# Optimization experiments

Hardware: AMD Instinct MI355X
Metric: run time of the kernel (lower is better)

Reference implementation:

```python
import jax, jax.numpy as jnp
import numpy as np

N0, N1, E, B = 100000, 100000, 800000, 1024
F0, F1 = 93, 43


def _gin(x, src, dst, w, b, n):
    # GINConv(eps=0): h_i = Lin(x_i + sum_{j->i} x_j)
    agg = jax.ops.segment_sum(x[src], dst, num_segments=n)
    return (x + agg) @ w + b


def _pool(x, batch, num_graphs):
    s = jax.ops.segment_sum(x, batch, num_segments=num_graphs)
    cnt = jax.ops.segment_sum(jnp.ones((x.shape[0],), x.dtype), batch, num_segments=num_graphs)
    mean = s / jnp.maximum(cnt, 1.0)[:, None]
    mx = jax.ops.segment_max(x, batch, num_segments=num_graphs)
    return jnp.concatenate([mean, mx], axis=1)


def _pairnorm(x, eps=1e-5):
    x = x - x.mean(axis=0, keepdims=True)
    return x / jnp.sqrt(eps + (x * x).sum(-1).mean())


def _bn(x, gamma, beta, eps=1e-5):
    mu = x.mean(axis=0, keepdims=True)
    var = x.var(axis=0, keepdims=True)
    return (x - mu) / jnp.sqrt(var + eps) * gamma + beta


def _branch(x, ei, batch, n, wc_a, bc_a, wc_b, bc_b, fg_w1, fg_b1, fg_w2, fg_b2, fg_g, fg_bt, ff_w1, ff_b1, ff_w2, ff_b2):
    src, dst = ei[0], ei[1]
    h = jax.nn.relu(_gin(x, src, dst, wc_a, bc_a, n))
    h = jax.nn.relu(_gin(h, src, dst, wc_b, bc_b, n))
    g = _pairnorm(_pool(h, batch, B))
    g = jax.nn.relu(g @ fg_w1 + fg_b1)
    g = _bn(g @ fg_w2 + fg_b2, fg_g, fg_bt)  # [B, 512]
    z = jax.nn.relu(g @ ff_w1 + ff_b1)
    z = jax.nn.sigmoid(z @ ff_w2 + ff_b2)  # [B, 2]
    return z[:, 0], z[:, 1], g


def setup_inputs() -> dict:
    key = jax.random.key(0)
    ks = iter(jax.random.split(key, 40))

    def lin(fan_in, fan_out):
        bnd = 1.0 / np.sqrt(fan_in)
        w = jax.random.uniform(next(ks), (fan_in, fan_out), jnp.float32, -bnd, bnd)
        b = jax.random.uniform(next(ks), (fan_out,), jnp.float32, -bnd, bnd)
        return w, b

    x0 = jax.random.normal(next(ks), (N0, F0), jnp.float32)
    x1 = jax.random.normal(next(ks), (N1, F1), jnp.float32)
    ei0 = jax.random.randint(next(ks), (2, E), 0, N0, jnp.int32)
    ei1 = jax.random.randint(next(ks), (2, E), 0, N1, jnp.int32)
    b0 = jnp.sort(jax.random.randint(next(ks), (N0,), 0, B, jnp.int32))
    b1 = jnp.sort(jax.random.randint(next(ks), (N1,), 0, B, jnp.int32))

    inp = {"x0": x0, "edge_index_0": ei0, "batch_0": b0, "x1": x1, "edge_index_1": ei1, "batch_1": b1}
    inp["w_c1"], inp["b_c1"] = lin(F0, F0)
    inp["w_c2"], inp["b_c2"] = lin(F0, F0 * 10)
    inp["w_c3"], inp["b_c3"] = lin(F1, F1)
    inp["w_c4"], inp["b_c4"] = lin(F1, F1 * 10)
    inp["fg0_w1"], inp["fg0_b1"] = lin(F0 * 10 * 2, 1024)
    inp["fg0_w2"], inp["fg0_b2"] = lin(1024, 512)
    inp["fg0_g"], inp["fg0_bt"] = jnp.ones((512,), jnp.float32), jnp.zeros((512,), jnp.float32)
    inp["fg1_w1"], inp["fg1_b1"] = lin(F1 * 10 * 2, 1024)
    inp["fg1_w2"], inp["fg1_b2"] = lin(1024, 512)
    inp["fg1_g"], inp["fg1_bt"] = jnp.ones((512,), jnp.float32), jnp.zeros((512,), jnp.float32)
    inp["ff0_w1"], inp["ff0_b1"] = lin(512, 256)
    inp["ff0_w2"], inp["ff0_b2"] = lin(256, 2)
    inp["ff1_w1"], inp["ff1_b1"] = lin(512, 256)
    inp["ff1_w2"], inp["ff1_b2"] = lin(256, 2)
    return inp


def reference(x0, edge_index_0, batch_0, x1, edge_index_1, batch_1,
              w_c1, b_c1, w_c2, b_c2, w_c3, b_c3, w_c4, b_c4,
              fg0_w1, fg0_b1, fg0_w2, fg0_b2, fg0_g, fg0_bt,
              fg1_w1, fg1_b1, fg1_w2, fg1_b2, fg1_g, fg1_bt,
              ff0_w1, ff0_b1, ff0_w2, ff0_b2,
              ff1_w1, ff1_b1, ff1_w2, ff1_b2):
    alpha, beta, xg0 = _branch(x0, edge_index_0, batch_0, N0, w_c1, b_c1, w_c2, b_c2,
                               fg0_w1, fg0_b1, fg0_w2, fg0_b2, fg0_g, fg0_bt,
                               ff0_w1, ff0_b1, ff0_w2, ff0_b2)
    alpha1, beta1, xg1 = _branch(x1, edge_index_1, batch_1, N1, w_c3, b_c3, w_c4, b_c4,
                                 fg1_w1, fg1_b1, fg1_w2, fg1_b2, fg1_g, fg1_bt,
                                 ff1_w1, ff1_b1, ff1_w2, ff1_b2)
    return (alpha, beta, xg0, xg1, alpha1, beta1)
```

## Files before the change

### kernel.cpp

```cpp
#include <hip/hip_runtime.h>
#include <hip/hip_bf16.h>
#include <math.h>

#define EDGES 800000
#define NNODES 100000
#define NGRAPH 1024

typedef __attribute__((ext_vector_type(8))) short short8v;
typedef __attribute__((ext_vector_type(4))) float float4v;
typedef unsigned short ushort_t;

__device__ inline ushort_t f2bf(float f) {
  __hip_bfloat16 h = __float2bfloat16(f);
  return *reinterpret_cast<ushort_t*>(&h);
}
__device__ inline float bf2f(ushort_t u) {
  return __uint_as_float(((unsigned int)u) << 16);
}

#define NBMAX 512

__global__ __launch_bounds__(256) void bcount_k(const int* __restrict__ dst,
                                                int* __restrict__ bcnt, int E,
                                                int NB) {
  __shared__ int hist[NBMAX];
  int t = threadIdx.x;
  for (int b = t; b < NB; b += 256) hist[b] = 0;
  __syncthreads();
  int e0 = blockIdx.x * 4096;
  int e1 = min(E, e0 + 4096);
  for (int e = e0 + t; e < e1; e += 256) atomicAdd(&hist[dst[e] >> 8], 1);
  __syncthreads();
  for (int b = t; b < NB; b += 256)
    if (hist[b] > 0) atomicAdd(&bcnt[b], hist[b]);
}

__global__ __launch_bounds__(512) void bscan_k(const int* __restrict__ bcnt,
                                               int* __restrict__ boff, int NB) {
  __shared__ int tmp[512];
  int t = threadIdx.x;
  int v = (t < NB) ? bcnt[t] : 0;
  tmp[t] = v;
  __syncthreads();
  for (int off = 1; off < 512; off <<= 1) {
    int x = (t >= off) ? tmp[t - off] : 0;
    __syncthreads();
    tmp[t] += x;
    __syncthreads();
  }
  if (t < NB) boff[t] = tmp[t] - v;
  if (t == NB - 1) boff[NB] = tmp[t];
}

__global__ __launch_bounds__(256) void bscatter_k(const int* __restrict__ src,
                                                  const int* __restrict__ dst,
                                                  const int* __restrict__ boff,
                                                  int* __restrict__ bcur,
                                                  int2* __restrict__ EB, int E,
                                                  int NB) {
  __shared__ int hist[NBMAX], run[NBMAX], lcur[NBMAX];
  int t = threadIdx.x;
  for (int b = t; b < NB; b += 256) {
    hist[b] = 0;
    lcur[b] = 0;
  }
  __syncthreads();
  int e0 = blockIdx.x * 4096;
  int e1 = min(E, e0 + 4096);
  for (int e = e0 + t; e < e1; e += 256) atomicAdd(&hist[dst[e] >> 8], 1);
  __syncthreads();
  for (int b = t; b < NB; b += 256)
    if (hist[b] > 0) run[b] = atomicAdd(&bcur[b], hist[b]);
  __syncthreads();
  for (int e = e0 + t; e < e1; e += 256) {
    int d = dst[e];
    int b = d >> 8;
    int l = atomicAdd(&lcur[b], 1);
    int pos = boff[b] + run[b] + l;
    EB[pos] = make_int2(src[e], d);
  }
}

__global__ __launch_bounds__(256) void bucket_csr_k(const int2* __restrict__ EB,
                                                    const int* __restrict__ boff,
                                                    int* __restrict__ rowstart,
                                                    int* __restrict__ adj, int N,
                                                    int NB, int E) {
  __shared__ int cnt[256], pfx[256], lcur[256];
  int b = blockIdx.x, t = threadIdx.x;
  int e0 = boff[b], e1 = boff[b + 1];
  cnt[t] = 0;
  __syncthreads();
  for (int e = e0 + t; e < e1; e += 256) atomicAdd(&cnt[EB[e].y & 255], 1);
  __syncthreads();
  int v = cnt[t];
  pfx[t] = v;
  __syncthreads();
  for (int off = 1; off < 256; off <<= 1) {
    int x = (t >= off) ? pfx[t - off] : 0;
    __syncthreads();
    pfx[t] += x;
    __syncthreads();
  }
  int node = (b << 8) + t;
  if (node < N) rowstart[node] = e0 + pfx[t] - v;
  if (b == NB - 1 && t == 0) rowstart[N] = E;
  lcur[t] = 0;
  __syncthreads();
  for (int e = e0 + t; e < e1; e += 256) {
    int2 ed = EB[e];
    int ln = ed.y & 255;
    int l = atomicAdd(&lcur[ln], 1);
    adj[e0 + pfx[ln] - cnt[ln] + l] = ed.x;
  }
}

__global__ __launch_bounds__(256) void gstart_k(const int* __restrict__ bat,
                                                int* __restrict__ gs, int N, int B) {
  int g = blockIdx.x * 256 + threadIdx.x;
  if (g > B) return;
  if (g == B) {
    gs[B] = N;
    return;
  }
  int lo = 0, hi = N;
  while (lo < hi) {
    int mid = (lo + hi) >> 1;
    if (bat[mid] < g) lo = mid + 1;
    else hi = mid;
  }
  gs[g] = lo;
}

template <int KP>
__global__ __launch_bounds__(256) void tobf16_k(const float* __restrict__ x,
                                                ushort_t* __restrict__ out, int M,
                                                int F) {
  long i = (long)blockIdx.x * 256 + threadIdx.x;
  if (i >= (long)M * KP) return;
  int r = (int)(i / KP), c = (int)(i % KP);
  float v = (c < F) ? x[(long)r * F + c] : 0.f;
  out[i] = f2bf(v);
}

template <int KP>
__global__ __launch_bounds__(256) void gather_k(const ushort_t* __restrict__ X,
                                                const int* __restrict__ rowstart,
                                                const int* __restrict__ adj,
                                                ushort_t* __restrict__ out, int M) {
  constexpr int CH = KP / 8;
  long tid = (long)blockIdx.x * 256 + threadIdx.x;
  if (tid >= (long)M * CH) return;
  int node = (int)(tid / CH), ch = (int)(tid % CH);
  int o = ch * 8;
  float acc[8];
  uint4 self = *(const uint4*)&X[(long)node * KP + o];
  {
    const unsigned int u[4] = {self.x, self.y, self.z, self.w};
#pragma unroll
    for (int i = 0; i < 4; ++i) {
      acc[2 * i] = __uint_as_float((u[i] & 0xFFFFu) << 16);
      acc[2 * i + 1] = __uint_as_float(u[i] & 0xFFFF0000u);
    }
  }
  auto add4 = [&](uint4 v) {
    const unsigned int u[4] = {v.x, v.y, v.z, v.w};
#pragma unroll
    for (int i = 0; i < 4; ++i) {
      acc[2 * i] += __uint_as_float((u[i] & 0xFFFFu) << 16);
      acc[2 * i + 1] += __uint_as_float(u[i] & 0xFFFF0000u);
    }
  };
  int rs = rowstart[node], re = rowstart[node + 1];
  int e = rs;
  for (; e + 4 <= re; e += 4) {
    int j0 = adj[e], j1 = adj[e + 1], j2 = adj[e + 2], j3 = adj[e + 3];
    uint4 v0 = *(const uint4*)&X[(long)j0 * KP + o];
    uint4 v1 = *(const uint4*)&X[(long)j1 * KP + o];
    uint4 v2 = *(const uint4*)&X[(long)j2 * KP + o];
    uint4 v3 = *(const uint4*)&X[(long)j3 * KP + o];
    add4(v0);
    add4(v1);
    add4(v2);
    add4(v3);
  }
  for (; e < re; ++e) {
    int j = adj[e];
    add4(*(const uint4*)&X[(long)j * KP + o]);
  }
  uint4 r;
  unsigned int* p = &r.x;
#pragma unroll
  for (int i = 0; i < 4; ++i) {
    unsigned int lo = f2bf(acc[2 * i]);
    unsigned int hi = f2bf(acc[2 * i + 1]);
    p[i] = lo | (hi << 16);
  }
  *(uint4*)&out[(long)node * KP + o] = r;
}

__global__ __launch_bounds__(256) void wt_k(const float* __restrict__ W,
                                            ushort_t* __restrict__ WT, int K, int N,
                                            int KP, int Npad) {
  int i = blockIdx.x * 256 + threadIdx.x;
  if (i >= Npad * KP) return;
  int n = i / KP, k = i % KP;
  float v = (k < K && n < N) ? W[(long)k * N + n] : 0.f;
  WT[i] = f2bf(v);
}

template <int KP>
__global__ __launch_bounds__(256) void conv_gemm2_k(
    const ushort_t* __restrict__ A, const ushort_t* __restrict__ WT,
    const float* __restrict__ bias, ushort_t* __restrict__ Cout, int M, int Nc,
    int OW, int NT) {
  constexpr int NKS = KP / 32;
  int tid = threadIdx.x;
  int wid = tid >> 6, lane = tid & 63;
  int lr = lane & 15, q = lane >> 4;
  int lk = q * 8;
  int row0 = blockIdx.x * 64;
  int arow = row0 + wid * 16 + lr;

  short8v a[NKS];
  const ushort_t* ap = A + (long)arow * KP + lk;
#pragma unroll
  for (int ks = 0; ks < NKS; ++ks) a[ks] = *(const short8v*)(ap + ks * 32);

  for (int ct = 0; ct < NT; ++ct) {
    int col0 = ct * 64;
    float4v acc[4];
#pragma unroll
    for (int i = 0; i < 4; ++i) acc[i] = (float4v){0.f, 0.f, 0.f, 0.f};
#pragma unroll
    for (int ks = 0; ks < NKS; ++ks) {
#pragma unroll
      for (int nf = 0; nf < 4; ++nf) {
        short8v b =
            *(const short8v*)&WT[(long)(col0 + nf * 16 + lr) * KP + ks * 32 + lk];
        acc[nf] = __builtin_amdgcn_mfma_f32_16x16x32_bf16(a[ks], b, acc[nf], 0, 0, 0);
      }
    }
#pragma unroll
    for (int nf = 0; nf < 4; ++nf) {
      int gc = col0 + nf * 16 + lr;
      if (gc >= OW) continue;
      float bv = (gc < Nc) ? bias[gc] : 0.f;
#pragma unroll
      for (int i = 0; i < 4; ++i) {
        int gr = row0 + wid * 16 + q * 4 + i;
        if (gr < M) {
          float v = (gc < Nc) ? fmaxf(acc[nf][i] + bv, 0.f) : 0.f;
          Cout[(long)gr * OW + gc] = f2bf(v);
        }
      }
    }
  }
}

template <int KP>
__global__ __launch_bounds__(64) void conv_pool2_k(
    const ushort_t* __restrict__ A, const ushort_t* __restrict__ WT,
    const float* __restrict__ bias, const int* __restrict__ gstart,
    float* __restrict__ pool, int Nc, int NCpool) {
  constexpr int NKS = KP / 32;
  int g = blockIdx.x;
  int col0 = blockIdx.y * 64;
  int rs = gstart[g], re = gstart[g + 1];
  int rows = re - rs;
  int lane = threadIdx.x;
  int lr = lane & 15, q = lane >> 4, lk = q * 8;

  short8v bfr[NKS][4];
  float bv[4];
#pragma unroll
  for (int nf = 0; nf < 4; ++nf) {
    int gc = col0 + nf * 16 + lr;
    bv[nf] = (gc < Nc) ? bias[gc] : 0.f;
#pragma unroll
    for (int ks = 0; ks < NKS; ++ks)
      bfr[ks][nf] = *(const short8v*)&WT[(long)gc * KP + ks * 32 + lk];
  }

  float wsum[4][4] = {}, wmax[4][4] = {};
  int nch = (rows + 15) >> 4;
  int rem = rows & 15;
  const ushort_t* ap = A + (long)(rs + lr) * KP + lk;

  short8v a0[NKS], a1[NKS];
  if (nch > 0) {
#pragma unroll
    for (int ks = 0; ks < NKS; ++ks) a0[ks] = *(const short8v*)(ap + ks * 32);
  }
  for (int c = 0; c < nch; ++c) {
    const ushort_t* apn = ap + (long)16 * KP;
    if (c + 1 < nch) {
#pragma unroll
      for (int ks = 0; ks < NKS; ++ks) a1[ks] = *(const short8v*)(apn + ks * 32);
    }
    float4v acc[4];
#pragma unroll
    for (int nf = 0; nf < 4; ++nf)
      acc[nf] = (float4v){bv[nf], bv[nf], bv[nf], bv[nf]};
#pragma unroll
    for (int ks = 0; ks < NKS; ++ks)
#pragma unroll
      for (int nf = 0; nf < 4; ++nf)
        acc[nf] = __builtin_amdgcn_mfma_f32_16x16x32_bf16(a0[ks], bfr[ks][nf],
                                                          acc[nf], 0, 0, 0);
    bool tail = (c == nch - 1) && (rem != 0);
    if (!tail) {
#pragma unroll
      for (int i = 0; i < 4; ++i)
#pragma unroll
        for (int nf = 0; nf < 4; ++nf) {
          float v = fmaxf(acc[nf][i], 0.f);
          wsum[nf][i] += v;
          wmax[nf][i] = fmaxf(wmax[nf][i], v);
        }
    } else {
#pragma unroll
      for (int i = 0; i < 4; ++i) {
        bool ok = (q * 4 + i) < rem;
#pragma unroll
        for (int nf = 0; nf < 4; ++nf) {
          float v = ok ? fmaxf(acc[nf][i], 0.f) : 0.f;
          wsum[nf][i] += v;
          wmax[nf][i] = fmaxf(wmax[nf][i], v);
        }
      }
    }
#pragma unroll
    for (int ks = 0; ks < NKS; ++ks) a0[ks] = a1[ks];
    ap = apn;
  }

  float inv = 1.f / fmaxf((float)rows, 1.f);
#pragma unroll
  for (int nf = 0; nf < 4; ++nf) {
    float s = (wsum[nf][0] + wsum[nf][1]) + (wsum[nf][2] + wsum[nf][3]);
    float m = fmaxf(fmaxf(wmax[nf][0], wmax[nf][1]),
                    fmaxf(wmax[nf][2], wmax[nf][3]));
    s += __shfl_xor(s, 16);
    s += __shfl_xor(s, 32);
    m = fmaxf(m, __shfl_xor(m, 16));
    m = fmaxf(m, __shfl_xor(m, 32));
    int gc = col0 + nf * 16 + lr;
    if (q == 0 && gc < Nc) {
      pool[(long)g * 2 * NCpool + gc] = s * inv;
      pool[(long)g * 2 * NCpool + NCpool + gc] = m;
    }
  }
}

__global__ __launch_bounds__(256) void fc_mfma_k(const ushort_t* __restrict__ A,
                                                 const ushort_t* __restrict__ WT,
                                                 float* __restrict__ PART, int KP,
                                                 int Nc, int Kc) {
  int tid = threadIdx.x;
  int wid = tid >> 6, lane = tid & 63;
  int lr = lane & 15, q = lane >> 4, lk = q * 8;
  int row0 = blockIdx.y * 64, col0 = blockIdx.x * 64;
  int M = gridDim.y * 64;
  int kbeg = blockIdx.z * Kc;
  int arow = row0 + wid * 16 + lr;
  const ushort_t* ap = A + (long)arow * KP + kbeg + lk;
  const ushort_t* wp = WT + (long)col0 * KP + kbeg + lk;

  float4v acc[4];
#pragma unroll
  for (int i = 0; i < 4; ++i) acc[i] = (float4v){0.f, 0.f, 0.f, 0.f};

  for (int k0 = 0; k0 < Kc; k0 += 32) {
    short8v a = *(const short8v*)(ap + k0);
#pragma unroll
    for (int nf = 0; nf < 4; ++nf) {
      short8v b = *(const short8v*)(wp + (long)(nf * 16 + lr) * KP + k0);
      acc[nf] = __builtin_amdgcn_mfma_f32_16x16x32_bf16(a, b, acc[nf], 0, 0, 0);
    }
  }

  float* P = PART + (long)blockIdx.z * M * Nc;
#pragma unroll
  for (int nf = 0; nf < 4; ++nf) {
    int gc = col0 + nf * 16 + lr;
#pragma unroll
    for (int i = 0; i < 4; ++i) {
      int gr = row0 + wid * 16 + q * 4 + i;
      P[(long)gr * Nc + gc] = acc[nf][i];
    }
  }
}

__global__ __launch_bounds__(256) void sk_epi2_k(const float* __restrict__ PART,
                                                 const float* __restrict__ bias,
                                                 float* __restrict__ Cf,
                                                 ushort_t* __restrict__ Cb, int M,
                                                 int Nc, int SK, int relu) {
  long idx = (long)blockIdx.x * 256 + threadIdx.x;
  if (idx >= (long)M * Nc) return;
  int c = (int)(idx % Nc);
  float s = bias[c];
  for (int z = 0; z < SK; ++z) s += PART[(long)z * M * Nc + idx];
  if (relu) s = fmaxf(s, 0.f);
  if (Cf) Cf[idx] = s;
  if (Cb) Cb[idx] = f2bf(s);
}

__global__ __launch_bounds__(256) void colstat_part_k(const float* __restrict__ X,
                                                      float* __restrict__ PS,
                                                      float* __restrict__ ssqtot,
                                                      int Rows, int Cols, int CR) {
  __shared__ float sred[256];
  int c0 = blockIdx.x * 64;
  int chunk = blockIdx.y;
  int t = threadIdx.x;
  int c = c0 + (t & 63);
  int rg = t >> 6;
  int rbeg = chunk * CR, rend = min(Rows, rbeg + CR);
  float s = 0.f, s2 = 0.f;
  if (c < Cols) {
    for (int r = rbeg + rg; r < rend; r += 4) {
      float v = X[(long)r * Cols + c];
      s += v;
      s2 += v * v;
    }
  }
  sred[t] = s;
  __syncthreads();
  if (t < 64 && c0 + t < Cols)
    PS[(long)chunk * Cols + c0 + t] = sred[t] + sred[t + 64] + sred[t + 128] + sred[t + 192];
  for (int off = 32; off > 0; off >>= 1) s2 += __shfl_down(s2, off);
  if ((t & 63) == 0) atomicAdd(ssqtot, s2);
}

__global__ __launch_bounds__(256) void colstat_fin_k(const float* __restrict__ PS,
                                                     float* __restrict__ cm, int Rows,
                                                     int Cols, int nchunk) {
  int c = blockIdx.x * 256 + threadIdx.x;
  if (c >= Cols) return;
  float s = 0.f;
  for (int z = 0; z < nchunk; ++z) s += PS[(long)z * Cols + c];
  cm[c] = s / Rows;
}

__global__ __launch_bounds__(256) void pn_scale_k(const float* __restrict__ cm,
                                                  const float* __restrict__ ssqtot,
                                                  float* __restrict__ scale, int Rows,
                                                  int Cols) {
  __shared__ float red[256];
  int t = threadIdx.x;
  float s = 0.f;
  for (int i = t; i < Cols; i += 256) {
    float v = cm[i];
    s += v * v;
  }
  red[t] = s;
  __syncthreads();
  for (int off = 128; off > 0; off >>= 1) {
    if (t < off) red[t] += red[t + off];
    __syncthreads();
  }
  if (t == 0) {
    float ssq = ssqtot[0] - (float)Rows * red[0];
    scale[0] = 1.f / sqrtf(1e-5f + ssq / Rows);
  }
}

__global__ __launch_bounds__(256) void pn_apply2_k(const float* __restrict__ X,
                                                   const float* __restrict__ cm,
                                                   const float* __restrict__ scale,
                                                   ushort_t* __restrict__ outB,
                                                   int Rows, int Cols, int KP1) {
  long idx = (long)blockIdx.x * 256 + threadIdx.x;
  if (idx >= (long)Rows * KP1) return;
  int r = (int)(idx / KP1), c = (int)(idx % KP1);
  float v = 0.f;
  if (c < Cols) v = (X[(long)r * Cols + c] - cm[c]) * scale[0];
  outB[idx] = f2bf(v);
}

__global__ __launch_bounds__(256) void bn_part_k(const float* __restrict__ X,
                                                 float* __restrict__ PS,
                                                 float* __restrict__ PQ, int Rows,
                                                 int Cols, int CR) {
  __shared__ float s1[256], s2l[256];
  int c0 = blockIdx.x * 64;
  int chunk = blockIdx.y;
  int t = threadIdx.x;
  int c = c0 + (t & 63);
  int rg = t >> 6;
  int rbeg = chunk * CR, rend = min(Rows, rbeg + CR);
  float a = 0.f, b = 0.f;
  if (c < Cols) {
    for (int r = rbeg + rg; r < rend; r += 4) {
      float v = X[(long)r * Cols + c];
      a += v;
      b += v * v;
    }
  }
  s1[t] = a;
  s2l[t] = b;
  __syncthreads();
  if (t < 64 && c0 + t < Cols) {
    PS[(long)chunk * Cols + c0 + t] = s1[t] + s1[t + 64] + s1[t + 128] + s1[t + 192];
    PQ[(long)chunk * Cols + c0 + t] = s2l[t] + s2l[t + 64] + s2l[t + 128] + s2l[t + 192];
  }
}

__global__ __launch_bounds__(256) void bn_fin_k(const float* __restrict__ PS,
                                                const float* __restrict__ PQ,
                                                float* __restrict__ mu,
                                                float* __restrict__ var, int Rows,
                                                int Cols, int nchunk) {
  int c = blockIdx.x * 256 + threadIdx.x;
  if (c >= Cols) return;
  float s = 0.f, q = 0.f;
  for (int z = 0; z < nchunk; ++z) {
    s += PS[(long)z * Cols + c];
    q += PQ[(long)z * Cols + c];
  }
  float m = s / Rows;
  mu[c] = m;
  var[c] = q / Rows - m * m;
}

__global__ void bn_apply2_k(float* __restrict__ X, const float* __restrict__ mu,
                            const float* __restrict__ var, const float* __restrict__ g,
                            const float* __restrict__ b, ushort_t* __restrict__ XB16,
                            int Rows, int Cols) {
  long idx = (long)blockIdx.x * 256 + threadIdx.x;
  if (idx >= (long)Rows * Cols) return;
  int c = (int)(idx % Cols);
  float v = (X[idx] - mu[c]) / sqrtf(var[c] + 1e-5f) * g[c] + b[c];
  X[idx] = v;
  XB16[idx] = f2bf(v);
}

__global__ __launch_bounds__(64) void ff2_k(const ushort_t* __restrict__ Z,
                                            const float* __restrict__ W2,
                                            const float* __restrict__ b2,
                                            float* __restrict__ alpha,
                                            float* __restrict__ beta, int K) {
  int row = blockIdx.x;
  int t = threadIdx.x;
  float s0 = 0.f, s1 = 0.f;
  for (int k = t; k < K; k += 64) {
    float z = bf2f(Z[(long)row * K + k]);
    s0 += z * W2[2 * k];
    s1 += z * W2[2 * k + 1];
  }
  for (int off = 32; off > 0; off >>= 1) {
    s0 += __shfl_down(s0, off);
    s1 += __shfl_down(s1, off);
  }
  if (t == 0) {
    alpha[row] = 1.f / (1.f + expf(-(s0 + b2[0])));
    beta[row] = 1.f / (1.f + expf(-(s1 + b2[1])));
  }
}

template <int KP>
static void run_branch(const float* x, const int* ei, const int* bat,
                       const float* wc1, const float* bc1, const float* wc2,
                       const float* bc2, const float* fgw1, const float* fgb1,
                       const float* fgw2, const float* fgb2, const float* fgg,
                       const float* fgbt, const float* ffw1, const float* ffb1,
                       const float* ffw2, const float* ffb2, int N, int F,
                       float* out_alpha, float* out_beta, float* out_xg,
                       ushort_t* XB, ushort_t* XA, ushort_t* H, ushort_t* WT,
                       int* rowstart, int* BC, int* boff, int* adj, int* GS,
                       float* POOL, float* CM, float* MU, float* VAR, float* SSQ,
                       float* PSUM, float* PSQ, ushort_t* POOLB, ushort_t* WTF1,
                       ushort_t* WTF2, ushort_t* WTFF, ushort_t* G1B, ushort_t* XGB,
                       ushort_t* Z1B, float* PART, hipStream_t stream) {
  const int NC = F * 10;
  const int Bn = NGRAPH;
  const int* src = ei;
  const int* dst = ei + EDGES;
  const int MB = (N + 63) / 64;
  const int Mpad = MB * 64;
  const int NB = (N + 255) >> 8;

  int2* EB = (int2*)XB;
  int* bcnt = BC;
  int* bcur = BC + NBMAX;
  hipMemsetAsync(BC, 0, 2 * NBMAX * 4, stream);
  bcount_k<<<(EDGES + 4095) / 4096, 256, 0, stream>>>(dst, bcnt, EDGES, NB);
  bscan_k<<<1, 512, 0, stream>>>(bcnt, boff, NB);
  bscatter_k<<<(EDGES + 4095) / 4096, 256, 0, stream>>>(src, dst, boff, bcur, EB, EDGES, NB);
  bucket_csr_k<<<NB, 256, 0, stream>>>(EB, boff, rowstart, adj, N, NB, EDGES);
  gstart_k<<<(NGRAPH + 256) / 256, 256, 0, stream>>>(bat, GS, N, NGRAPH);

  constexpr int CH = KP / 8;
  if (Mpad > N)
    hipMemsetAsync(XA + (size_t)N * KP, 0, (size_t)(Mpad - N) * KP * 2, stream);
  tobf16_k<KP><<<(int)(((long)N * KP + 255) / 256), 256, 0, stream>>>(x, XB, N, F);
  gather_k<KP><<<(int)(((long)N * CH + 255) / 256), 256, 0, stream>>>(XB, rowstart, adj, XA, N);
  wt_k<<<(((F + 63) / 64) * 64 * KP + 255) / 256, 256, 0, stream>>>(
      wc1, WT, F, F, KP, ((F + 63) / 64) * 64);
  conv_gemm2_k<KP><<<MB, 256, 0, stream>>>(XA, WT, bc1, H, N, F, KP, (KP + 63) / 64);
  gather_k<KP><<<(int)(((long)N * CH + 255) / 256), 256, 0, stream>>>(H, rowstart, adj, XA, N);
  int Npad2 = ((NC + 63) / 64) * 64;
  wt_k<<<(Npad2 * KP + 255) / 256, 256, 0, stream>>>(wc2, WT, F, NC, KP, Npad2);
  conv_pool2_k<KP><<<dim3(NGRAPH, Npad2 / 64), 64, 0, stream>>>(XA, WT, bc2, GS, POOL, NC, NC);

  int Cols = 2 * NC;
  const int NCH = 16, CR = NGRAPH / NCH;
  hipMemsetAsync(SSQ, 0, 8, stream);
  colstat_part_k<<<dim3((Cols + 63) / 64, NCH), 256, 0, stream>>>(POOL, PSUM, SSQ, Bn, Cols, CR);
  colstat_fin_k<<<(Cols + 255) / 256, 256, 0, stream>>>(PSUM, CM, Bn, Cols, NCH);
  pn_scale_k<<<1, 256, 0, stream>>>(CM, SSQ, SSQ + 1, Bn, Cols);

  int KP1 = ((Cols + 127) / 128) * 128;
  pn_apply2_k<<<(int)(((long)Bn * KP1 + 255) / 256), 256, 0, stream>>>(
      POOL, CM, SSQ + 1, POOLB, Bn, Cols, KP1);
  wt_k<<<(1024 * KP1 + 255) / 256, 256, 0, stream>>>(fgw1, WTF1, Cols, 1024, KP1, 1024);
  fc_mfma_k<<<dim3(16, 16, 4), 256, 0, stream>>>(POOLB, WTF1, PART, KP1, 1024, KP1 / 4);
  sk_epi2_k<<<(Bn * 1024 + 255) / 256, 256, 0, stream>>>(PART, fgb1, nullptr, G1B, Bn, 1024, 4, 1);
  wt_k<<<(512 * 1024 + 255) / 256, 256, 0, stream>>>(fgw2, WTF2, 1024, 512, 1024, 512);
  fc_mfma_k<<<dim3(8, 16, 4), 256, 0, stream>>>(G1B, WTF2, PART, 1024, 512, 256);
  sk_epi2_k<<<(Bn * 512 + 255) / 256, 256, 0, stream>>>(PART, fgb2, out_xg, nullptr, Bn, 512, 4, 0);
  bn_part_k<<<dim3(8, 8), 256, 0, stream>>>(out_xg, PSUM, PSQ, Bn, 512, 128);
  bn_fin_k<<<2, 256, 0, stream>>>(PSUM, PSQ, MU, VAR, Bn, 512, 8);
  bn_apply2_k<<<(Bn * 512 + 255) / 256, 256, 0, stream>>>(out_xg, MU, VAR, fgg, fgbt, XGB, Bn, 512);
  wt_k<<<(256 * 512 + 255) / 256, 256, 0, stream>>>(ffw1, WTFF, 512, 256, 512, 256);
  fc_mfma_k<<<dim3(4, 16, 8), 256, 0, stream>>>(XGB, WTFF, PART, 512, 256, 64);
  sk_epi2_k<<<(Bn * 256 + 255) / 256, 256, 0, stream>>>(PART, ffb1, nullptr, Z1B, Bn, 256, 8, 1);
  ff2_k<<<Bn, 64, 0, stream>>>(Z1B, ffw2, ffb2, out_alpha, out_beta, 256);
}

extern "C" void kernel_launch(void* const* d_in, const int* in_sizes, int n_in,
                              void* d_out, int out_size, void* d_ws, size_t ws_size,
                              hipStream_t stream) {
  if (n_in < 34) return;
  const float* x0 = (const float*)d_in[0];
  const int* ei0 = (const int*)d_in[1];
  const int* b0 = (const int*)d_in[2];
  const float* x1 = (const float*)d_in[3];
  const int* ei1 = (const int*)d_in[4];
  const int* b1 = (const int*)d_in[5];
  const float* w_c1 = (const float*)d_in[6];
  const float* b_c1 = (const float*)d_in[7];
  const float* w_c2 = (const float*)d_in[8];
  const float* b_c2 = (const float*)d_in[9];
  const float* w_c3 = (const float*)d_in[10];
  const float* b_c3 = (const float*)d_in[11];
  const float* w_c4 = (const float*)d_in[12];
  const float* b_c4 = (const float*)d_in[13];
  const float* fg0_w1 = (const float*)d_in[14];
  const float* fg0_b1 = (const float*)d_in[15];
  const float* fg0_w2 = (const float*)d_in[16];
  const float* fg0_b2 = (const float*)d_in[17];
  const float* fg0_g = (const float*)d_in[18];
  const float* fg0_bt = (const float*)d_in[19];
  const float* fg1_w1 = (const float*)d_in[20];
  const float* fg1_b1 = (const float*)d_in[21];
  const float* fg1_w2 = (const float*)d_in[22];
  const float* fg1_b2 = (const float*)d_in[23];
  const float* fg1_g = (const float*)d_in[24];
  const float* fg1_bt = (const float*)d_in[25];
  const float* ff0_w1 = (const float*)d_in[26];
  const float* ff0_b1 = (const float*)d_in[27];
  const float* ff0_w2 = (const float*)d_in[28];
  const float* ff0_b2 = (const float*)d_in[29];
  const float* ff1_w1 = (const float*)d_in[30];
  const float* ff1_b1 = (const float*)d_in[31];
  const float* ff1_w2 = (const float*)d_in[32];
  const float* ff1_b2 = (const float*)d_in[33];

  float* out = (float*)d_out;
  float* alpha = out;
  float* beta = out + 1024;
  float* xg0 = out + 2048;
  float* xg1 = out + 2048 + 1024 * 512;
  float* alpha1 = out + 2048 + 2 * 1024 * 512;
  float* beta1 = alpha1 + 1024;

  char* w = (char*)d_ws;
  auto alloc = [&](size_t bytes) -> void* {
    void* p = (void*)w;
    w += ((bytes + 255) / 256) * 256;
    return p;
  };
  const int Mpad = ((NNODES + 63) / 64) * 64;
  ushort_t* XB = (ushort_t*)alloc((size_t)Mpad * 96 * 2);
  ushort_t* XA = (ushort_t*)alloc((size_t)Mpad * 96 * 2);
  ushort_t* H = (ushort_t*)alloc((size_t)Mpad * 96 * 2);
  ushort_t* WT = (ushort_t*)alloc((size_t)960 * 96 * 2);
  int* rowstart = (int*)alloc((size_t)(NNODES + 1) * 4);
  int* BC = (int*)alloc(2 * NBMAX * 4);
  int* boff = (int*)alloc((NBMAX + 1) * 4);
  int* adj = (int*)alloc((size_t)EDGES * 4);
  int* GS = (int*)alloc((size_t)(NGRAPH + 1) * 4);
  float* POOL = (float*)alloc((size_t)NGRAPH * 1860 * 4);
  float* CM = (float*)alloc(1860 * 4);
  float* MU = (float*)alloc(512 * 4);
  float* VAR = (float*)alloc(512 * 4);
  float* SSQ = (float*)alloc(256);
  float* PSUM = (float*)alloc((size_t)16 * 1920 * 4);
  float* PSQ = (float*)alloc((size_t)8 * 512 * 4);
  ushort_t* POOLB = (ushort_t*)alloc((size_t)NGRAPH * 1920 * 2);
  ushort_t* WTF1 = (ushort_t*)alloc((size_t)1024 * 1920 * 2);
  ushort_t* WTF2 = (ushort_t*)alloc((size_t)512 * 1024 * 2);
  ushort_t* WTFF = (ushort_t*)alloc((size_t)256 * 512 * 2);
  ushort_t* G1B = (ushort_t*)alloc((size_t)NGRAPH * 1024 * 2);
  ushort_t* XGB = (ushort_t*)alloc((size_t)NGRAPH * 512 * 2);
  ushort_t* Z1B = (ushort_t*)alloc((size_t)NGRAPH * 256 * 2);
  if ((size_t)(w - (char*)d_ws) > ws_size) return;

  float* PART = (float*)XB;

  run_branch<96>(x0, ei0, b0, w_c1, b_c1, w_c2, b_c2, fg0_w1, fg0_b1, fg0_w2,
                 fg0_b2, fg0_g, fg0_bt, ff0_w1, ff0_b1, ff0_w2, ff0_b2, NNODES,
                 93, alpha, beta, xg0, XB, XA, H, WT, rowstart, BC, boff, adj, GS,
                 POOL, CM, MU, VAR, SSQ, PSUM, PSQ, POOLB, WTF1, WTF2, WTFF, G1B,
                 XGB, Z1B, PART, stream);
  run_branch<64>(x1, ei1, b1, w_c3, b_c3, w_c4, b_c4, fg1_w1, fg1_b1, fg1_w2,
                 fg1_b2, fg1_g, fg1_bt, ff1_w1, ff1_b1, ff1_w2, ff1_b2, NNODES,
                 43, alpha1, beta1, xg1, XB, XA, H, WT, rowstart, BC, boff, adj,
                 GS, POOL, CM, MU, VAR, SSQ, PSUM, PSQ, POOLB, WTF1, WTF2, WTFF,
                 G1B, XGB, Z1B, PART, stream);
}
```

Baseline: 599.0 us.

## Tile weight transposes through shared memory, prefetch FC operands, simplify pool reduction

Replaces the naive per-element weight transpose with a 64x64 shared-memory tiled transpose, so both the float reads and the bf16 writes are coalesced. The FC MFMA kernel now double-buffers its A and B fragment loads one k-step ahead, overlapping global loads with MFMA issue. The fused conv+pool kernel keeps one sum/max accumulator per column fragment instead of four, which cuts register use. The transpose kernels are small relative to the graph gather work, so the overall effect is likely modest.

```diff
diff --git a/kernel.cpp b/kernel.cpp
--- a/kernel.cpp
+++ b/kernel.cpp
@@ -199,14 +199,25 @@
   *(uint4*)&out[(long)node * KP + o] = r;
 }
 
-__global__ __launch_bounds__(256) void wt_k(const float* __restrict__ W,
-                                            ushort_t* __restrict__ WT, int K, int N,
-                                            int KP, int Npad) {
-  int i = blockIdx.x * 256 + threadIdx.x;
-  if (i >= Npad * KP) return;
-  int n = i / KP, k = i % KP;
-  float v = (k < K && n < N) ? W[(long)k * N + n] : 0.f;
-  WT[i] = f2bf(v);
+__global__ __launch_bounds__(256) void wt2_k(const float* __restrict__ W,
+                                             ushort_t* __restrict__ WT, int K, int N,
+                                             int KP, int Npad) {
+  __shared__ ushort_t tile[64][66];
+  int t = threadIdx.x;
+  int tx = t & 63, ty = t >> 6;
+  int n0 = blockIdx.x * 64, k0 = blockIdx.y * 64;
+#pragma unroll
+  for (int kk = ty; kk < 64; kk += 4) {
+    int k = k0 + kk, n = n0 + tx;
+    float v = (k < K && n < N) ? W[(long)k * N + n] : 0.f;
+    tile[kk][tx] = f2bf(v);
+  }
+  __syncthreads();
+#pragma unroll
+  for (int nn = ty; nn < 64; nn += 4) {
+    int n = n0 + nn, k = k0 + tx;
+    if (n < Npad && k < KP) WT[(long)n * KP + k] = tile[tx][nn];
+  }
 }
 
 template <int KP>
@@ -282,7 +293,7 @@
       bfr[ks][nf] = *(const short8v*)&WT[(long)gc * KP + ks * 32 + lk];
   }
 
-  float wsum[4][4] = {}, wmax[4][4] = {};
+  float wsums[4] = {}, wmaxs[4] = {};
   int nch = (rows + 15) >> 4;
   int rem = rows & 15;
   const ushort_t* ap = A + (long)(rs + lr) * KP + lk;
@@ -311,23 +322,22 @@
     bool tail = (c == nch - 1) && (rem != 0);
     if (!tail) {
 #pragma unroll
-      for (int i = 0; i < 4; ++i)
-#pragma unroll
-        for (int nf = 0; nf < 4; ++nf) {
-          float v = fmaxf(acc[nf][i], 0.f);
-          wsum[nf][i] += v;
-          wmax[nf][i] = fmaxf(wmax[nf][i], v);
-        }
+      for (int nf = 0; nf < 4; ++nf) {
+        float r0 = fmaxf(acc[nf][0], 0.f), r1 = fmaxf(acc[nf][1], 0.f);
+        float r2 = fmaxf(acc[nf][2], 0.f), r3 = fmaxf(acc[nf][3], 0.f);
+        wsums[nf] += (r0 + r1) + (r2 + r3);
+        wmaxs[nf] = fmaxf(wmaxs[nf], fmaxf(fmaxf(acc[nf][0], acc[nf][1]),
+                                           fmaxf(acc[nf][2], acc[nf][3])));
+      }
     } else {
 #pragma unroll
-      for (int i = 0; i < 4; ++i) {
-        bool ok = (q * 4 + i) < rem;
-#pragma unroll
-        for (int nf = 0; nf < 4; ++nf) {
-          float v = ok ? fmaxf(acc[nf][i], 0.f) : 0.f;
-          wsum[nf][i] += v;
-          wmax[nf][i] = fmaxf(wmax[nf][i], v);
-        }
+      for (int nf = 0; nf < 4; ++nf) {
+        float v[4];
+#pragma unroll
+        for (int i = 0; i < 4; ++i)
+          v[i] = ((q * 4 + i) < rem) ? fmaxf(acc[nf][i], 0.f) : 0.f;
+        wsums[nf] += (v[0] + v[1]) + (v[2] + v[3]);
+        wmaxs[nf] = fmaxf(wmaxs[nf], fmaxf(fmaxf(v[0], v[1]), fmaxf(v[2], v[3])));
       }
     }
 #pragma unroll
@@ -338,9 +348,8 @@
   float inv = 1.f / fmaxf((float)rows, 1.f);
 #pragma unroll
   for (int nf = 0; nf < 4; ++nf) {
-    float s = (wsum[nf][0] + wsum[nf][1]) + (wsum[nf][2] + wsum[nf][3]);
-    float m = fmaxf(fmaxf(wmax[nf][0], wmax[nf][1]),
-                    fmaxf(wmax[nf][2], wmax[nf][3]));
+    float s = wsums[nf];
+    float m = wmaxs[nf];
     s += __shfl_xor(s, 16);
     s += __shfl_xor(s, 32);
     m = fmaxf(m, __shfl_xor(m, 16));
@@ -365,19 +374,33 @@
   int kbeg = blockIdx.z * Kc;
   int arow = row0 + wid * 16 + lr;
   const ushort_t* ap = A + (long)arow * KP + kbeg + lk;
-  const ushort_t* wp = WT + (long)col0 * KP + kbeg + lk;
+  const ushort_t* wp = WT + (long)(col0 + lr) * KP + kbeg + lk;
 
   float4v acc[4];
 #pragma unroll
   for (int i = 0; i < 4; ++i) acc[i] = (float4v){0.f, 0.f, 0.f, 0.f};
 
+  short8v a0 = *(const short8v*)ap;
+  short8v b0[4];
+#pragma unroll
+  for (int nf = 0; nf < 4; ++nf)
+    b0[nf] = *(const short8v*)(wp + (long)(nf * 16) * KP);
+
   for (int k0 = 0; k0 < Kc; k0 += 32) {
-    short8v a = *(const short8v*)(ap + k0);
-#pragma unroll
-    for (int nf = 0; nf < 4; ++nf) {
-      short8v b = *(const short8v*)(wp + (long)(nf * 16 + lr) * KP + k0);
-      acc[nf] = __builtin_amdgcn_mfma_f32_16x16x32_bf16(a, b, acc[nf], 0, 0, 0);
-    }
+    short8v a1;
+    short8v b1[4];
+    if (k0 + 32 < Kc) {
+      a1 = *(const short8v*)(ap + k0 + 32);
+#pragma unroll
+      for (int nf = 0; nf < 4; ++nf)
+        b1[nf] = *(const short8v*)(wp + (long)(nf * 16) * KP + k0 + 32);
+    }
+#pragma unroll
+    for (int nf = 0; nf < 4; ++nf)
+      acc[nf] = __builtin_amdgcn_mfma_f32_16x16x32_bf16(a0, b0[nf], acc[nf], 0, 0, 0);
+    a0 = a1;
+#pragma unroll
+    for (int nf = 0; nf < 4; ++nf) b0[nf] = b1[nf];
   }
 
   float* P = PART + (long)blockIdx.z * M * Nc;
@@ -581,6 +604,7 @@
   const int MB = (N + 63) / 64;
   const int Mpad = MB * 64;
   const int NB = (N + 255) >> 8;
+  const int KT = (KP + 63) / 64;
 
   int2* EB = (int2*)XB;
   int* bcnt = BC;
@@ -596,13 +620,13 @@
   if (Mpad > N)
     hipMemsetAsync(XA + (size_t)N * KP, 0, (size_t)(Mpad - N) * KP * 2, stream);
   tobf16_k<KP><<<(int)(((long)N * KP + 255) / 256), 256, 0, stream>>>(x, XB, N, F);
+  int Fpad = ((F + 63) / 64) * 64;
   gather_k<KP><<<(int)(((long)N * CH + 255) / 256), 256, 0, stream>>>(XB, rowstart, adj, XA, N);
-  wt_k<<<(((F + 63) / 64) * 64 * KP + 255) / 256, 256, 0, stream>>>(
-      wc1, WT, F, F, KP, ((F + 63) / 64) * 64);
-  conv_gemm2_k<KP><<<MB, 256, 0, stream>>>(XA, WT, bc1, H, N, F, KP, (KP + 63) / 64);
+  wt2_k<<<dim3(Fpad / 64, KT), 256, 0, stream>>>(wc1, WT, F, F, KP, Fpad);
+  conv_gemm2_k<KP><<<MB, 256, 0, stream>>>(XA, WT, bc1, H, N, F, KP, KT);
   gather_k<KP><<<(int)(((long)N * CH + 255) / 256), 256, 0, stream>>>(H, rowstart, adj, XA, N);
   int Npad2 = ((NC + 63) / 64) * 64;
-  wt_k<<<(Npad2 * KP + 255) / 256, 256, 0, stream>>>(wc2, WT, F, NC, KP, Npad2);
+  wt2_k<<<dim3(Npad2 / 64, KT), 256, 0, stream>>>(wc2, WT, F, NC, KP, Npad2);
   conv_pool2_k<KP><<<dim3(NGRAPH, Npad2 / 64), 64, 0, stream>>>(XA, WT, bc2, GS, POOL, NC, NC);
 
   int Cols = 2 * NC;
@@ -615,16 +639,16 @@
   int KP1 = ((Cols + 127) / 128) * 128;
   pn_apply2_k<<<(int)(((long)Bn * KP1 + 255) / 256), 256, 0, stream>>>(
       POOL, CM, SSQ + 1, POOLB, Bn, Cols, KP1);
-  wt_k<<<(1024 * KP1 + 255) / 256, 256, 0, stream>>>(fgw1, WTF1, Cols, 1024, KP1, 1024);
+  wt2_k<<<dim3(1024 / 64, KP1 / 64), 256, 0, stream>>>(fgw1, WTF1, Cols, 1024, KP1, 1024);
   fc_mfma_k<<<dim3(16, 16, 4), 256, 0, stream>>>(POOLB, WTF1, PART, KP1, 1024, KP1 / 4);
   sk_epi2_k<<<(Bn * 1024 + 255) / 256, 256, 0, stream>>>(PART, fgb1, nullptr, G1B, Bn, 1024, 4, 1);
-  wt_k<<<(512 * 1024 + 255) / 256, 256, 0, stream>>>(fgw2, WTF2, 1024, 512, 1024, 512);
+  wt2_k<<<dim3(512 / 64, 1024 / 64), 256, 0, stream>>>(fgw2, WTF2, 1024, 512, 1024, 512);
   fc_mfma_k<<<dim3(8, 16, 4), 256, 0, stream>>>(G1B, WTF2, PART, 1024, 512, 256);
   sk_epi2_k<<<(Bn * 512 + 255) / 256, 256, 0, stream>>>(PART, fgb2, out_xg, nullptr, Bn, 512, 4, 0);
   bn_part_k<<<dim3(8, 8), 256, 0, stream>>>(out_xg, PSUM, PSQ, Bn, 512, 128);
   bn_fin_k<<<2, 256, 0, stream>>>(PSUM, PSQ, MU, VAR, Bn, 512, 8);
   bn_apply2_k<<<(Bn * 512 + 255) / 256, 256, 0, stream>>>(out_xg, MU, VAR, fgg, fgbt, XGB, Bn, 512);
-  wt_k<<<(256 * 512 + 255) / 256, 256, 0, stream>>>(ffw1, WTFF, 512, 256, 512, 256);
+  wt2_k<<<dim3(256 / 64, 512 / 64), 256, 0, stream>>>(ffw1, WTFF, 512, 256, 512, 256);
   fc_mfma_k<<<dim3(4, 16, 8), 256, 0, stream>>>(XGB, WTFF, PART, 512, 256, 64);
   sk_epi2_k<<<(Bn * 256 + 255) / 256, 256, 0, stream>>>(PART, ffb1, nullptr, Z1B, Bn, 256, 8, 1);
   ff2_k<<<Bn, 64, 0, stream>>>(Z1B, ffw2, ffb2, out_alpha, out_beta, 256);
```

Measured after the change: 630.0 us. 1.05x slower.
